# Kernel optimization log

Measured on AMD Instinct MI355X. Metric: run time of the kernel, lower is better.

## Reference

```python
import jax, jax.numpy as jnp
import numpy as np

B, C, L = 8, 256, 2048
G = min(C // 4, 32)  # 32 groups
EPS = 1e-6


def group_norm(x, gamma, beta):
    # x: (B, C, L)
    xg = x.reshape(B, G, C // G, L)
    mean = xg.mean(axis=(2, 3), keepdims=True)
    var = xg.var(axis=(2, 3), keepdims=True)
    xn = ((xg - mean) * jax.lax.rsqrt(var + EPS)).reshape(B, C, L)
    return xn * gamma[None, :, None] + beta[None, :, None]


def nin(h, w, b):
    # 1x1 projection over channel dim: (B,C,L),(C,D)->(B,D,L)
    return jnp.einsum('bcl,cd->bdl', h, w) + b[None, :, None]


def setup_inputs() -> dict:
    key = jax.random.key(0)
    ks = jax.random.split(key, 10)
    s = 1.0 / np.sqrt(C)
    return {
        'x': jax.random.normal(ks[0], (B, C, L), dtype=jnp.float32),
        'gn_gamma': jnp.ones((C,), jnp.float32),
        'gn_beta': jnp.zeros((C,), jnp.float32),
        'w0': jax.random.normal(ks[1], (C, C), jnp.float32) * s,
        'b0': jnp.zeros((C,), jnp.float32),
        'w1': jax.random.normal(ks[2], (C, C), jnp.float32) * s,
        'b1': jnp.zeros((C,), jnp.float32),
        'w2': jax.random.normal(ks[3], (C, C), jnp.float32) * s,
        'b2': jnp.zeros((C,), jnp.float32),
        'w3': jax.random.normal(ks[4], (C, C), jnp.float32) * s,
        'b3': jnp.zeros((C,), jnp.float32),
    }


def reference(x, gn_gamma, gn_beta, w0, b0, w1, b1, w2, b2, w3, b3):
    h = group_norm(x, gn_gamma, gn_beta)
    q = nin(h, w0, b0)
    k = nin(h, w1, b1)
    v = nin(h, w2, b2)
    # attention scores over the L dim, scaled by 1/sqrt(C)
    w = jnp.einsum('bcl,bci->bli', q, k) * (C ** -0.5)  # (B, L, L)
    w = jax.nn.softmax(w, axis=-1)
    h = jnp.einsum('bli,bci->bcl', w, v)
    h = nin(h, w3, b3)
    return x + h  # skip_rescale=False
```

## Files before the change

kernel.cpp:

```cpp
#include <hip/hip_runtime.h>

#define B_ 8
#define C_ 256
#define L_ 2048
#define G_ 32
static constexpr long CL = (long)C_ * L_;
static constexpr long LL = (long)L_ * L_;

typedef __attribute__((ext_vector_type(8))) short bf16x8;
typedef __attribute__((ext_vector_type(4))) float f32x4;

__device__ __forceinline__ ushort f2bf(float f) {
    union { float f; unsigned u; } v; v.f = f;
    unsigned r = v.u + 0x7FFFu + ((v.u >> 16) & 1u);
    return (ushort)(r >> 16);
}
__device__ __forceinline__ float bf2f(ushort u) {
    union { unsigned u; float f; } v; v.u = (unsigned)u << 16;
    return v.f;
}

__device__ __forceinline__ void ld16(const ushort* g, ushort* l) {
    __builtin_amdgcn_global_load_lds(
        (const __attribute__((address_space(1))) unsigned int*)g,
        (__attribute__((address_space(3))) unsigned int*)l, 16, 0, 0);
}

__device__ __forceinline__ int swz8(int bid, int nwg) {
    return (bid & 7) * (nwg >> 3) + (bid >> 3);
}

template<int OP>
__device__ __forceinline__ float blockReduce(float v) {
    __shared__ float tmp[4];
    int lane = threadIdx.x & 63;
    int w    = threadIdx.x >> 6;
#pragma unroll
    for (int off = 32; off; off >>= 1) {
        float o = __shfl_down(v, off);
        v = OP ? fmaxf(v, o) : (v + o);
    }
    if (lane == 0) tmp[w] = v;
    __syncthreads();
    float r = OP ? fmaxf(fmaxf(tmp[0], tmp[1]), fmaxf(tmp[2], tmp[3]))
                 : (tmp[0] + tmp[1] + tmp[2] + tmp[3]);
    __syncthreads();
    return r;
}

__global__ __launch_bounds__(256) void gn_t_kernel(const float* __restrict__ x,
                                                   const float* __restrict__ gamma,
                                                   const float* __restrict__ beta,
                                                   ushort* __restrict__ hb) {
    int bg = blockIdx.x;
    int b  = bg >> 5, g = bg & 31;
    const float* xg = x + (long)bg * 16384;
    const float4* xv = (const float4*)xg;
    float s = 0.f, ss = 0.f;
    for (int i = threadIdx.x; i < 4096; i += 256) {
        float4 v = xv[i];
        s  += v.x + v.y + v.z + v.w;
        ss += v.x * v.x + v.y * v.y + v.z * v.z + v.w * v.w;
    }
    s  = blockReduce<0>(s);
    ss = blockReduce<0>(ss);
    float mean = s * (1.f / 16384.f);
    float var  = ss * (1.f / 16384.f) - mean * mean;
    float rstd = rsqrtf(var + 1e-6f);
    float a[8], bb[8];
#pragma unroll
    for (int cc = 0; cc < 8; ++cc) {
        int c = g * 8 + cc;
        a[cc]  = gamma[c] * rstd;
        bb[cc] = beta[c] - mean * a[cc];
    }
    ushort* hp = hb + (long)b * CL + g * 8;
    for (int l = threadIdx.x; l < 2048; l += 256) {
        ushort o[8];
#pragma unroll
        for (int cc = 0; cc < 8; ++cc)
            o[cc] = f2bf(xg[cc * 2048 + l] * a[cc] + bb[cc]);
        *(uint4*)&hp[(long)l * 256] = *(uint4*)o;
    }
}

__global__ void transpose_w(const float* __restrict__ w0, const float* __restrict__ w1,
                            const float* __restrict__ w2, const float* __restrict__ w3,
                            ushort* __restrict__ wT4) {
    int which = blockIdx.y;
    const float* w = which == 0 ? w0 : which == 1 ? w1 : which == 2 ? w2 : w3;
    int d = blockIdx.x, c = threadIdx.x;
    wT4[which * 65536 + d * 256 + c] = f2bf(w[c * 256 + d]);
}

template<int TM, int TN>
__device__ __forceinline__ void gemm_body(const ushort* __restrict__ Mop,
                                          const ushort* __restrict__ Nop,
                                          long lda, long ldb, int K,
                                          ushort* As, ushort* Bs,
                                          f32x4 (&acc)[TM / 32][TN / 32]) {
    const int tid = threadIdx.x, lane = tid & 63, w = tid >> 6;
    const int r8 = lane >> 3, s8 = lane & 7;
    constexpr int CA = TM / 32, CB = TN / 32;
    for (int k0 = 0; k0 < K; k0 += 64) {
#pragma unroll
        for (int i = 0; i < CA; ++i) {
            int c   = w * CA + i;
            int row = c * 8 + r8;
            int ko  = (s8 ^ (row & 7)) << 3;
            ld16(Mop + (long)row * lda + k0 + ko, As + c * 512);
        }
#pragma unroll
        for (int i = 0; i < CB; ++i) {
            int c   = w * CB + i;
            int row = c * 8 + r8;
            int ko  = (s8 ^ (row & 7)) << 3;
            ld16(Nop + (long)row * ldb + k0 + ko, Bs + c * 512);
        }
        __syncthreads();
        const int wr = w >> 1, wc = w & 1;
#pragma unroll
        for (int kh = 0; kh < 2; ++kh) {
            int g = kh * 4 + (lane >> 4);
            bf16x8 av[TM / 32], bv[TN / 32];
#pragma unroll
            for (int mi = 0; mi < TM / 32; ++mi) {
                int row = wr * (TM / 2) + mi * 16 + (lane & 15);
                av[mi] = *(const bf16x8*)&As[row * 64 + ((g ^ (row & 7)) << 3)];
            }
#pragma unroll
            for (int ni = 0; ni < TN / 32; ++ni) {
                int row = wc * (TN / 2) + ni * 16 + (lane & 15);
                bv[ni] = *(const bf16x8*)&Bs[row * 64 + ((g ^ (row & 7)) << 3)];
            }
#pragma unroll
            for (int mi = 0; mi < TM / 32; ++mi)
#pragma unroll
                for (int ni = 0; ni < TN / 32; ++ni)
                    acc[mi][ni] = __builtin_amdgcn_mfma_f32_16x16x32_bf16(av[mi], bv[ni], acc[mi][ni], 0, 0, 0);
        }
        __syncthreads();
    }
}

#define GEMM_PROLOGUE(TM, TN)                                 \
    __shared__ ushort As[TM * 64];                            \
    __shared__ ushort Bs[TN * 64];                            \
    f32x4 acc[TM / 32][TN / 32];                              \
    _Pragma("unroll") for (int i = 0; i < TM / 32; ++i)       \
        _Pragma("unroll") for (int j = 0; j < TN / 32; ++j)   \
            _Pragma("unroll") for (int e = 0; e < 4; ++e) acc[i][j][e] = 0.f; \
    const int lane = threadIdx.x & 63, wv = threadIdx.x >> 6; \
    const int wr = wv >> 1, wc = wv & 1;

__global__ __launch_bounds__(256) void qkv_gemm(const ushort* __restrict__ wT4,
                                                const ushort* __restrict__ hb,
                                                ushort* __restrict__ qb,
                                                ushort* __restrict__ kb,
                                                ushort* __restrict__ vb,
                                                const float* __restrict__ bq,
                                                const float* __restrict__ bk,
                                                const float* __restrict__ bv_) {
    GEMM_PROLOGUE(128, 128)
    int l = swz8(blockIdx.x, 768);
    int xn = l & 1, ym = (l >> 1) & 15, z = l >> 5;
    int which = z % 3, b = z / 3;
    int m0 = ym * 128, n0 = xn * 128;
    gemm_body<128, 128>(hb + (long)b * CL + (long)m0 * 256,
                        wT4 + which * 65536 + (long)n0 * 256, 256, 256, 256, As, Bs, acc);
    const float* bias = which == 0 ? bq : which == 1 ? bk : bv_;
    ushort* outp = (which == 0 ? qb : which == 1 ? kb : vb) + (long)b * CL;
#pragma unroll
    for (int mi = 0; mi < 4; ++mi) {
        int mb = m0 + wr * 64 + mi * 16 + (lane >> 4) * 4;
#pragma unroll
        for (int ni = 0; ni < 4; ++ni) {
            int n = n0 + wc * 64 + ni * 16 + (lane & 15);
            float bval = bias[n];
            if (which < 2) {
#pragma unroll
                for (int r = 0; r < 4; ++r)
                    outp[(long)(mb + r) * 256 + n] = f2bf(acc[mi][ni][r] + bval);
            } else {
                ushort o[4];
#pragma unroll
                for (int r = 0; r < 4; ++r) o[r] = f2bf(acc[mi][ni][r] + bval);
                *(ushort4*)&outp[(long)n * L_ + mb] = *(ushort4*)o;
            }
        }
    }
}

__global__ __launch_bounds__(256) void score_gemm(const ushort* __restrict__ qb,
                                                  const ushort* __restrict__ kb,
                                                  ushort* __restrict__ S,
                                                  float* __restrict__ rs) {
    GEMM_PROLOGUE(128, 128)
    int l = swz8(blockIdx.x, 2048);
    int xn = l & 15, ym = (l >> 4) & 15, b = l >> 8;
    int m0 = ym * 128, n0 = xn * 128;
    gemm_body<128, 128>(qb + (long)b * CL + (long)m0 * 256,
                        kb + (long)b * CL + (long)n0 * 256, 256, 256, 256, As, Bs, acc);
    ushort* Sp = S + (long)b * LL;
    const int slot = xn * 2 + wc;
#pragma unroll
    for (int mi = 0; mi < 4; ++mi) {
        int mb = m0 + wr * 64 + mi * 16 + (lane >> 4) * 4;
#pragma unroll
        for (int r = 0; r < 4; ++r) {
            float psum = 0.f;
#pragma unroll
            for (int ni = 0; ni < 4; ++ni) {
                int n = n0 + wc * 64 + ni * 16 + (lane & 15);
                float e = __expf(acc[mi][ni][r] * 0.0625f);
                ushort eb = f2bf(e);
                Sp[(long)(mb + r) * L_ + n] = eb;
                psum += bf2f(eb);
            }
#pragma unroll
            for (int off = 1; off <= 8; off <<= 1)
                psum += __shfl_xor(psum, off);
            if ((lane & 15) == 0)
                rs[((long)b * L_ + mb + r) * 32 + slot] = psum;
        }
    }
}

__global__ __launch_bounds__(256) void pv_gemm(const ushort* __restrict__ S,
                                               const ushort* __restrict__ vb,
                                               const float* __restrict__ rs,
                                               ushort* __restrict__ hh) {
    GEMM_PROLOGUE(64, 128)
    int l = swz8(blockIdx.x, 512);
    int xn = l & 1, ym = (l >> 1) & 31, b = l >> 6;
    int m0 = ym * 64, n0 = xn * 128;
    gemm_body<64, 128>(S + (long)b * LL + (long)m0 * L_,
                       vb + (long)b * CL + (long)n0 * L_, L_, L_, L_, As, Bs, acc);
    ushort* outp = hh + (long)b * CL;
#pragma unroll
    for (int mi = 0; mi < 2; ++mi) {
        int mb = m0 + wr * 32 + mi * 16 + (lane >> 4) * 4;
        float rinv[4];
#pragma unroll
        for (int r = 0; r < 4; ++r) {
            const float4* rp = (const float4*)&rs[((long)b * L_ + mb + r) * 32];
            float4 s0 = rp[0], s1 = rp[1], s2 = rp[2], s3 = rp[3];
            float4 s4 = rp[4], s5 = rp[5], s6 = rp[6], s7 = rp[7];
            float t = s0.x + s0.y + s0.z + s0.w + s1.x + s1.y + s1.z + s1.w
                    + s2.x + s2.y + s2.z + s2.w + s3.x + s3.y + s3.z + s3.w
                    + s4.x + s4.y + s4.z + s4.w + s5.x + s5.y + s5.z + s5.w
                    + s6.x + s6.y + s6.z + s6.w + s7.x + s7.y + s7.z + s7.w;
            rinv[r] = 1.f / t;
        }
#pragma unroll
        for (int ni = 0; ni < 4; ++ni) {
            int n = n0 + wc * 64 + ni * 16 + (lane & 15);
#pragma unroll
            for (int r = 0; r < 4; ++r)
                outp[(long)(mb + r) * 256 + n] = f2bf(acc[mi][ni][r] * rinv[r]);
        }
    }
}

__global__ __launch_bounds__(256) void final_gemm(const ushort* __restrict__ w3T,
                                                  const ushort* __restrict__ hh,
                                                  const float* __restrict__ x,
                                                  const float* __restrict__ b3,
                                                  float* __restrict__ outp) {
    GEMM_PROLOGUE(64, 128)
    int l = swz8(blockIdx.x, 512);
    int xn = l & 15, ym = (l >> 4) & 3, b = l >> 6;
    int m0 = ym * 64, n0 = xn * 128;
    gemm_body<64, 128>(w3T + (long)m0 * 256,
                       hh + (long)b * CL + (long)n0 * 256, 256, 256, 256, As, Bs, acc);
    const float* xr = x + (long)b * CL;
    float* op = outp + (long)b * CL;
#pragma unroll
    for (int mi = 0; mi < 2; ++mi) {
        int mb = m0 + wr * 32 + mi * 16 + (lane >> 4) * 4;
#pragma unroll
        for (int ni = 0; ni < 4; ++ni) {
            int n = n0 + wc * 64 + ni * 16 + (lane & 15);
#pragma unroll
            for (int r = 0; r < 4; ++r) {
                long idx = (long)(mb + r) * L_ + n;
                op[idx] = acc[mi][ni][r] + b3[mb + r] + xr[idx];
            }
        }
    }
}

extern "C" void kernel_launch(void* const* d_in, const int* in_sizes, int n_in,
                              void* d_out, int out_size, void* d_ws, size_t ws_size,
                              hipStream_t stream) {
    const float* x     = (const float*)d_in[0];
    const float* gamma = (const float*)d_in[1];
    const float* beta  = (const float*)d_in[2];
    const float* w0 = (const float*)d_in[3];
    const float* b0 = (const float*)d_in[4];
    const float* w1 = (const float*)d_in[5];
    const float* b1 = (const float*)d_in[6];
    const float* w2 = (const float*)d_in[7];
    const float* b2 = (const float*)d_in[8];
    const float* w3 = (const float*)d_in[9];
    const float* b3 = (const float*)d_in[10];
    float* out = (float*)d_out;

    unsigned char* p = (unsigned char*)d_ws;
    ushort* hb = (ushort*)p; p += (size_t)B_ * CL * 2;
    ushort* qb = (ushort*)p; p += (size_t)B_ * CL * 2;
    ushort* kb = (ushort*)p; p += (size_t)B_ * CL * 2;
    ushort* vb = (ushort*)p; p += (size_t)B_ * CL * 2;
    ushort* S  = (ushort*)p; p += (size_t)B_ * LL * 2;
    float*  rs = (float*)p;  p += (size_t)B_ * L_ * 32 * 4;
    ushort* wT4 = (ushort*)p;
    ushort* hh = hb;

    dim3 blk(256);

    transpose_w<<<dim3(256, 4), blk, 0, stream>>>(w0, w1, w2, w3, wT4);
    gn_t_kernel<<<B_ * G_, blk, 0, stream>>>(x, gamma, beta, hb);

    qkv_gemm<<<768, blk, 0, stream>>>(wT4, hb, qb, kb, vb, b0, b1, b2);

    score_gemm<<<2048, blk, 0, stream>>>(qb, kb, S, rs);

    pv_gemm<<<512, blk, 0, stream>>>(S, vb, rs, hh);

    final_gemm<<<512, blk, 0, stream>>>(wT4 + 3 * 65536, hh, x, b3, out);
}
```

Before: 194.0 us.

## Double-buffer PV GEMM LDS tiles and widen score GEMM to 256x128 tiles

Generalizes the GEMM body over the warp grid and adds a double-buffered LDS path. The path prefetches the next K-slab through global_load_lds while MFMAs run on the current one, and it is used for the long-K PV GEMM. The score GEMM moves to 256x128 tiles with 8 waves per 512-thread block, which halves the block count and raises reuse of K tiles. Double buffering doubles LDS use for PV, and the larger score blocks may lower occupancy.

```diff
diff --git a/kernel.cpp b/kernel.cpp
--- a/kernel.cpp
+++ b/kernel.cpp
@@ -93,65 +93,92 @@
     wT4[which * 65536 + d * 256 + c] = f2bf(w[c * 256 + d]);
 }
 
-template<int TM, int TN>
+template<int TM, int TN, int WR, int WC, bool DB>
 __device__ __forceinline__ void gemm_body(const ushort* __restrict__ Mop,
                                           const ushort* __restrict__ Nop,
                                           long lda, long ldb, int K,
                                           ushort* As, ushort* Bs,
-                                          f32x4 (&acc)[TM / 32][TN / 32]) {
+                                          f32x4 (&acc)[TM / (16 * WR)][TN / (16 * WC)]) {
+    constexpr int NW = WR * WC;
+    constexpr int CA = TM / (8 * NW), CB = TN / (8 * NW);
+    constexpr int FM = TM / (16 * WR), FN = TN / (16 * WC);
     const int tid = threadIdx.x, lane = tid & 63, w = tid >> 6;
     const int r8 = lane >> 3, s8 = lane & 7;
-    constexpr int CA = TM / 32, CB = TN / 32;
-    for (int k0 = 0; k0 < K; k0 += 64) {
+    const int wrr = w / WC, wcc = w % WC;
+
+    auto stage = [&](int buf, int k0) {
+        ushort* Ad = As + buf * (TM * 64);
+        ushort* Bd = Bs + buf * (TN * 64);
 #pragma unroll
         for (int i = 0; i < CA; ++i) {
-            int c   = w * CA + i;
-            int row = c * 8 + r8;
-            int ko  = (s8 ^ (row & 7)) << 3;
-            ld16(Mop + (long)row * lda + k0 + ko, As + c * 512);
+            int c = w * CA + i, row = c * 8 + r8;
+            int ko = (s8 ^ (row & 7)) << 3;
+            ld16(Mop + (long)row * lda + k0 + ko, Ad + c * 512);
         }
 #pragma unroll
         for (int i = 0; i < CB; ++i) {
-            int c   = w * CB + i;
-            int row = c * 8 + r8;
-            int ko  = (s8 ^ (row & 7)) << 3;
-            ld16(Nop + (long)row * ldb + k0 + ko, Bs + c * 512);
-        }
-        __syncthreads();
-        const int wr = w >> 1, wc = w & 1;
+            int c = w * CB + i, row = c * 8 + r8;
+            int ko = (s8 ^ (row & 7)) << 3;
+            ld16(Nop + (long)row * ldb + k0 + ko, Bd + c * 512);
+        }
+    };
+
+    auto compute = [&](int buf) {
+        const ushort* Ac = As + buf * (TM * 64);
+        const ushort* Bc = Bs + buf * (TN * 64);
 #pragma unroll
         for (int kh = 0; kh < 2; ++kh) {
             int g = kh * 4 + (lane >> 4);
-            bf16x8 av[TM / 32], bv[TN / 32];
-#pragma unroll
-            for (int mi = 0; mi < TM / 32; ++mi) {
-                int row = wr * (TM / 2) + mi * 16 + (lane & 15);
-                av[mi] = *(const bf16x8*)&As[row * 64 + ((g ^ (row & 7)) << 3)];
-            }
-#pragma unroll
-            for (int ni = 0; ni < TN / 32; ++ni) {
-                int row = wc * (TN / 2) + ni * 16 + (lane & 15);
-                bv[ni] = *(const bf16x8*)&Bs[row * 64 + ((g ^ (row & 7)) << 3)];
-            }
-#pragma unroll
-            for (int mi = 0; mi < TM / 32; ++mi)
-#pragma unroll
-                for (int ni = 0; ni < TN / 32; ++ni)
+            bf16x8 av[FM], bv[FN];
+#pragma unroll
+            for (int mi = 0; mi < FM; ++mi) {
+                int row = wrr * (TM / WR) + mi * 16 + (lane & 15);
+                av[mi] = *(const bf16x8*)&Ac[row * 64 + ((g ^ (row & 7)) << 3)];
+            }
+#pragma unroll
+            for (int ni = 0; ni < FN; ++ni) {
+                int row = wcc * (TN / WC) + ni * 16 + (lane & 15);
+                bv[ni] = *(const bf16x8*)&Bc[row * 64 + ((g ^ (row & 7)) << 3)];
+            }
+#pragma unroll
+            for (int mi = 0; mi < FM; ++mi)
+#pragma unroll
+                for (int ni = 0; ni < FN; ++ni)
                     acc[mi][ni] = __builtin_amdgcn_mfma_f32_16x16x32_bf16(av[mi], bv[ni], acc[mi][ni], 0, 0, 0);
         }
-        __syncthreads();
-    }
-}
-
-#define GEMM_PROLOGUE(TM, TN)                                 \
-    __shared__ ushort As[TM * 64];                            \
-    __shared__ ushort Bs[TN * 64];                            \
-    f32x4 acc[TM / 32][TN / 32];                              \
-    _Pragma("unroll") for (int i = 0; i < TM / 32; ++i)       \
-        _Pragma("unroll") for (int j = 0; j < TN / 32; ++j)   \
+    };
+
+    if constexpr (!DB) {
+        for (int k0 = 0; k0 < K; k0 += 64) {
+            stage(0, k0);
+            __syncthreads();
+            compute(0);
+            __syncthreads();
+        }
+    } else {
+        stage(0, 0);
+        asm volatile("s_waitcnt vmcnt(0)" ::: "memory");
+        __builtin_amdgcn_s_barrier();
+        int cur = 0;
+        for (int k0 = 0; k0 < K; k0 += 64) {
+            if (k0 + 64 < K) stage(cur ^ 1, k0 + 64);
+            compute(cur);
+            asm volatile("s_waitcnt vmcnt(0)" ::: "memory");
+            __builtin_amdgcn_s_barrier();
+            cur ^= 1;
+        }
+    }
+}
+
+#define GEMM_PROLOGUE(TM, TN, WR, WC, DBF)                    \
+    __shared__ ushort As[DBF * TM * 64];                      \
+    __shared__ ushort Bs[DBF * TN * 64];                      \
+    f32x4 acc[TM / (16 * WR)][TN / (16 * WC)];                \
+    _Pragma("unroll") for (int i = 0; i < TM / (16 * WR); ++i)     \
+        _Pragma("unroll") for (int j = 0; j < TN / (16 * WC); ++j) \
             _Pragma("unroll") for (int e = 0; e < 4; ++e) acc[i][j][e] = 0.f; \
     const int lane = threadIdx.x & 63, wv = threadIdx.x >> 6; \
-    const int wr = wv >> 1, wc = wv & 1;
+    const int wrr = wv / WC, wcc = wv % WC; (void)wrr; (void)wcc;
 
 __global__ __launch_bounds__(256) void qkv_gemm(const ushort* __restrict__ wT4,
                                                 const ushort* __restrict__ hb,
@@ -161,21 +188,22 @@
                                                 const float* __restrict__ bq,
                                                 const float* __restrict__ bk,
                                                 const float* __restrict__ bv_) {
-    GEMM_PROLOGUE(128, 128)
+    GEMM_PROLOGUE(128, 128, 2, 2, 1)
     int l = swz8(blockIdx.x, 768);
     int xn = l & 1, ym = (l >> 1) & 15, z = l >> 5;
     int which = z % 3, b = z / 3;
     int m0 = ym * 128, n0 = xn * 128;
-    gemm_body<128, 128>(hb + (long)b * CL + (long)m0 * 256,
-                        wT4 + which * 65536 + (long)n0 * 256, 256, 256, 256, As, Bs, acc);
+    gemm_body<128, 128, 2, 2, false>(hb + (long)b * CL + (long)m0 * 256,
+                                     wT4 + which * 65536 + (long)n0 * 256,
+                                     256, 256, 256, As, Bs, acc);
     const float* bias = which == 0 ? bq : which == 1 ? bk : bv_;
     ushort* outp = (which == 0 ? qb : which == 1 ? kb : vb) + (long)b * CL;
 #pragma unroll
     for (int mi = 0; mi < 4; ++mi) {
-        int mb = m0 + wr * 64 + mi * 16 + (lane >> 4) * 4;
+        int mb = m0 + wrr * 64 + mi * 16 + (lane >> 4) * 4;
 #pragma unroll
         for (int ni = 0; ni < 4; ++ni) {
-            int n = n0 + wc * 64 + ni * 16 + (lane & 15);
+            int n = n0 + wcc * 64 + ni * 16 + (lane & 15);
             float bval = bias[n];
             if (which < 2) {
 #pragma unroll
@@ -191,27 +219,28 @@
     }
 }
 
-__global__ __launch_bounds__(256) void score_gemm(const ushort* __restrict__ qb,
+__global__ __launch_bounds__(512) void score_gemm(const ushort* __restrict__ qb,
                                                   const ushort* __restrict__ kb,
                                                   ushort* __restrict__ S,
                                                   float* __restrict__ rs) {
-    GEMM_PROLOGUE(128, 128)
-    int l = swz8(blockIdx.x, 2048);
-    int xn = l & 15, ym = (l >> 4) & 15, b = l >> 8;
-    int m0 = ym * 128, n0 = xn * 128;
-    gemm_body<128, 128>(qb + (long)b * CL + (long)m0 * 256,
-                        kb + (long)b * CL + (long)n0 * 256, 256, 256, 256, As, Bs, acc);
+    GEMM_PROLOGUE(256, 128, 4, 2, 1)
+    int l = swz8(blockIdx.x, 1024);
+    int xn = l & 15, ym = (l >> 4) & 7, b = l >> 7;
+    int m0 = ym * 256, n0 = xn * 128;
+    gemm_body<256, 128, 4, 2, false>(qb + (long)b * CL + (long)m0 * 256,
+                                     kb + (long)b * CL + (long)n0 * 256,
+                                     256, 256, 256, As, Bs, acc);
     ushort* Sp = S + (long)b * LL;
-    const int slot = xn * 2 + wc;
+    const int slot = xn * 2 + wcc;
 #pragma unroll
     for (int mi = 0; mi < 4; ++mi) {
-        int mb = m0 + wr * 64 + mi * 16 + (lane >> 4) * 4;
+        int mb = m0 + wrr * 64 + mi * 16 + (lane >> 4) * 4;
 #pragma unroll
         for (int r = 0; r < 4; ++r) {
             float psum = 0.f;
 #pragma unroll
             for (int ni = 0; ni < 4; ++ni) {
-                int n = n0 + wc * 64 + ni * 16 + (lane & 15);
+                int n = n0 + wcc * 64 + ni * 16 + (lane & 15);
                 float e = __expf(acc[mi][ni][r] * 0.0625f);
                 ushort eb = f2bf(e);
                 Sp[(long)(mb + r) * L_ + n] = eb;
@@ -230,16 +259,17 @@
                                                const ushort* __restrict__ vb,
                                                const float* __restrict__ rs,
                                                ushort* __restrict__ hh) {
-    GEMM_PROLOGUE(64, 128)
+    GEMM_PROLOGUE(64, 128, 2, 2, 2)
     int l = swz8(blockIdx.x, 512);
     int xn = l & 1, ym = (l >> 1) & 31, b = l >> 6;
     int m0 = ym * 64, n0 = xn * 128;
-    gemm_body<64, 128>(S + (long)b * LL + (long)m0 * L_,
-                       vb + (long)b * CL + (long)n0 * L_, L_, L_, L_, As, Bs, acc);
+    gemm_body<64, 128, 2, 2, true>(S + (long)b * LL + (long)m0 * L_,
+                                   vb + (long)b * CL + (long)n0 * L_,
+                                   L_, L_, L_, As, Bs, acc);
     ushort* outp = hh + (long)b * CL;
 #pragma unroll
     for (int mi = 0; mi < 2; ++mi) {
-        int mb = m0 + wr * 32 + mi * 16 + (lane >> 4) * 4;
+        int mb = m0 + wrr * 32 + mi * 16 + (lane >> 4) * 4;
         float rinv[4];
 #pragma unroll
         for (int r = 0; r < 4; ++r) {
@@ -254,7 +284,7 @@
         }
 #pragma unroll
         for (int ni = 0; ni < 4; ++ni) {
-            int n = n0 + wc * 64 + ni * 16 + (lane & 15);
+            int n = n0 + wcc * 64 + ni * 16 + (lane & 15);
 #pragma unroll
             for (int r = 0; r < 4; ++r)
                 outp[(long)(mb + r) * 256 + n] = f2bf(acc[mi][ni][r] * rinv[r]);
@@ -267,20 +297,21 @@
                                                   const float* __restrict__ x,
                                                   const float* __restrict__ b3,
                                                   float* __restrict__ outp) {
-    GEMM_PROLOGUE(64, 128)
+    GEMM_PROLOGUE(64, 128, 2, 2, 1)
     int l = swz8(blockIdx.x, 512);
     int xn = l & 15, ym = (l >> 4) & 3, b = l >> 6;
     int m0 = ym * 64, n0 = xn * 128;
-    gemm_body<64, 128>(w3T + (long)m0 * 256,
-                       hh + (long)b * CL + (long)n0 * 256, 256, 256, 256, As, Bs, acc);
+    gemm_body<64, 128, 2, 2, false>(w3T + (long)m0 * 256,
+                                    hh + (long)b * CL + (long)n0 * 256,
+                                    256, 256, 256, As, Bs, acc);
     const float* xr = x + (long)b * CL;
     float* op = outp + (long)b * CL;
 #pragma unroll
     for (int mi = 0; mi < 2; ++mi) {
-        int mb = m0 + wr * 32 + mi * 16 + (lane >> 4) * 4;
+        int mb = m0 + wrr * 32 + mi * 16 + (lane >> 4) * 4;
 #pragma unroll
         for (int ni = 0; ni < 4; ++ni) {
-            int n = n0 + wc * 64 + ni * 16 + (lane & 15);
+            int n = n0 + wcc * 64 + ni * 16 + (lane & 15);
 #pragma unroll
             for (int r = 0; r < 4; ++r) {
                 long idx = (long)(mb + r) * L_ + n;
@@ -316,16 +347,14 @@
     ushort* wT4 = (ushort*)p;
     ushort* hh = hb;
 
-    dim3 blk(256);
-
-    transpose_w<<<dim3(256, 4), blk, 0, stream>>>(w0, w1, w2, w3, wT4);
-    gn_t_kernel<<<B_ * G_, blk, 0, stream>>>(x, gamma, beta, hb);
-
-    qkv_gemm<<<768, blk, 0, stream>>>(wT4, hb, qb, kb, vb, b0, b1, b2);
-
-    score_gemm<<<2048, blk, 0, stream>>>(qb, kb, S, rs);
-
-    pv_gemm<<<512, blk, 0, stream>>>(S, vb, rs, hh);
-
-    final_gemm<<<512, blk, 0, stream>>>(wT4 + 3 * 65536, hh, x, b3, out);
-}
+    transpose_w<<<dim3(256, 4), dim3(256), 0, stream>>>(w0, w1, w2, w3, wT4);
+    gn_t_kernel<<<B_ * G_, dim3(256), 0, stream>>>(x, gamma, beta, hb);
+
+    qkv_gemm<<<768, dim3(256), 0, stream>>>(wT4, hb, qb, kb, vb, b0, b1, b2);
+
+    score_gemm<<<1024, dim3(512), 0, stream>>>(qb, kb, S, rs);
+
+    pv_gemm<<<512, dim3(256), 0, stream>>>(S, vb, rs, hh);
+
+    final_gemm<<<512, dim3(256), 0, stream>>>(wT4 + 3 * 65536, hh, x, b3, out);
+}
```

Result: slower. 203.3 us (+4.8%).
